# Kernel optimization log

Hardware: AMD Instinct MI355X
Metric: run time of the kernel (lower is better)

## Reference

```python
import jax, jax.numpy as jnp
import numpy as np

B, N, D, H, S = 4, 32768, 256, 8, 64
DH = D // H  # 32


def setup_inputs() -> dict:
    key = jax.random.key(0)
    ks = jax.random.split(key, 8)
    s = 0.02
    return {
        "x": jax.random.normal(ks[0], (B, N, D), jnp.float32),
        "W_fx": jax.random.normal(ks[1], (D, D), jnp.float32) * s,
        "b_fx": jnp.zeros((D,), jnp.float32),
        "W_x": jax.random.normal(ks[2], (D, D), jnp.float32) * s,
        "b_x": jnp.zeros((D,), jnp.float32),
        "W_slice": jax.random.normal(ks[3], (DH, S), jnp.float32) * s,
        "b_slice": jnp.zeros((S,), jnp.float32),
        "temperature": jnp.full((1, H, 1, 1), 0.5, jnp.float32),
        "W_qkv": jax.random.normal(ks[4], (DH, 3 * DH), jnp.float32) * s,  # qkv_bias=False
        "W_out": jax.random.normal(ks[5], (D, D), jnp.float32) * s,
        "b_out": jnp.zeros((D,), jnp.float32),
    }


def reference(x, W_fx, b_fx, W_x, b_x, W_slice, b_slice, temperature, W_qkv, W_out, b_out):
    b, n, d = x.shape
    h, dh = H, d // H
    scale = dh ** -0.5
    # per-head projections: [b, h, n, dh]
    fx_mid = (x @ W_fx + b_fx).reshape(b, n, h, dh).transpose(0, 2, 1, 3)
    x_mid = (x @ W_x + b_x).reshape(b, n, h, dh).transpose(0, 2, 1, 3)
    # soft slice assignment: softmax over slices [b, h, n, s]
    logits = (x_mid @ W_slice + b_slice) / temperature
    slice_weights = jax.nn.softmax(logits, axis=-1)
    slice_norm = slice_weights.sum(axis=2)  # [b, h, s]
    # weighted pooling of points into slice tokens [b, h, s, dh]
    slice_token = jnp.einsum('bhnc,bhns->bhsc', fx_mid, slice_weights)
    slice_token = slice_token / (slice_norm[..., None] + 1e-5)
    # tiny attention among slice tokens
    q, k, v = jnp.split(slice_token @ W_qkv, 3, axis=-1)
    dots = jnp.einsum('bhsc,bhtc->bhst', q, k) * scale
    attn = jax.nn.softmax(dots, axis=-1)
    out_slice_token = attn @ v  # [b, h, s, dh]
    # scatter back to points [b, h, n, dh]
    out_x = jnp.einsum('bhsc,bhns->bhnc', out_slice_token, slice_weights)
    out_x = out_x.transpose(0, 2, 1, 3).reshape(b, n, d)
    return out_x @ W_out + b_out
```

## Files before the change

kernel.cpp:

```cpp
#include <hip/hip_runtime.h>
#include <math.h>

#define TS_N 32768
#define TS_M 131072

typedef short bf16x8 __attribute__((ext_vector_type(8)));
typedef float f32x4  __attribute__((ext_vector_type(4)));
typedef unsigned short us4 __attribute__((ext_vector_type(4)));
typedef unsigned short us8 __attribute__((ext_vector_type(8)));

static __device__ __forceinline__ unsigned short f2bf(float f) {
    unsigned u = __float_as_uint(f);
    u = u + 0x7FFF + ((u >> 16) & 1);
    return (unsigned short)(u >> 16);
}
static __device__ __forceinline__ float bf2f(unsigned short b) {
    return __uint_as_float(((unsigned)b) << 16);
}

#define GL16(gp, lp) __builtin_amdgcn_global_load_lds( \
    (const __attribute__((address_space(1))) unsigned int*)(gp), \
    (__attribute__((address_space(3))) unsigned int*)(lp), 16, 0, 0)

__global__ __launch_bounds__(256) void k0_split(
    const float* __restrict__ src, unsigned short* __restrict__ h,
    unsigned short* __restrict__ l, int n4)
{
    for (int i = blockIdx.x * 256 + threadIdx.x; i < n4; i += gridDim.x * 256) {
        float4 v = ((const float4*)src)[i];
        us4 vh, vl;
        float c[4] = {v.x, v.y, v.z, v.w};
#pragma unroll
        for (int j = 0; j < 4; ++j) {
            unsigned short hh = f2bf(c[j]);
            vh[j] = hh;
            vl[j] = f2bf(c[j] - bf2f(hh));
        }
        ((us4*)h)[i] = vh;
        ((us4*)l)[i] = vl;
    }
}

__global__ __launch_bounds__(256) void k0_wt(
    const float* __restrict__ Wfx, const float* __restrict__ Wx,
    unsigned short* __restrict__ Wth, unsigned short* __restrict__ Wtl)
{
    const int n = blockIdx.x;
    const int wsel = blockIdx.y;
    const int k = threadIdx.x;
    const float v = (wsel ? Wx : Wfx)[k * 256 + n];
    const unsigned short hh = f2bf(v);
    const int idx = (wsel * 256 + n) * 256 + k;
    Wth[idx] = hh;
    Wtl[idx] = f2bf(v - bf2f(hh));
}

template<int K>
static __device__ __forceinline__ void gemm_body(
    const unsigned short* __restrict__ Ah, const unsigned short* __restrict__ Al,
    const unsigned short* __restrict__ Bth, const unsigned short* __restrict__ Btl,
    const float* __restrict__ bias, float* __restrict__ OUT,
    int row0, int n0)
{
    __shared__ unsigned short Alds[2][128 * 32];
    __shared__ unsigned short Blds[2][128 * 32];
    const int t = threadIdx.x;
    const int w = t >> 6, l = t & 63;
    const int wm = w >> 1, wn = w & 1;
    const int lr = l & 15, lk = l >> 4;

    f32x4 acc[4][4];
#pragma unroll
    for (int i = 0; i < 4; ++i)
#pragma unroll
        for (int j = 0; j < 4; ++j) {
            acc[i][j][0] = 0.f; acc[i][j][1] = 0.f;
            acc[i][j][2] = 0.f; acc[i][j][3] = 0.f;
        }

    const int NSTEP = K / 32;
    for (int step = 0; step < NSTEP; ++step) {
        const int kk = step * 32;
        if (step > 0) __syncthreads();
#pragma unroll
        for (int g2i = 0; g2i < 2; ++g2i) {
            const int g2 = w + g2i * 4;
            const size_t ar = (size_t)(row0 + g2 * 16 + lr) * K + kk + lk * 8;
            const size_t br = (size_t)(g2 * 16 + lr) * K + kk + lk * 8;
            const int lb = g2 * 64 * 8;
            GL16(Ah + ar, &Alds[0][lb]);
            GL16(Al + ar, &Alds[1][lb]);
            GL16(Bth + br, &Blds[0][lb]);
            GL16(Btl + br, &Blds[1][lb]);
        }
        __syncthreads();

        bf16x8 ah[4], al[4], bh[4], bl[4];
#pragma unroll
        for (int g = 0; g < 4; ++g) {
            const int ac = (((wm * 4 + g) * 4 + lk) * 16 + lr) * 8;
            ah[g] = *(const bf16x8*)&Alds[0][ac];
            al[g] = *(const bf16x8*)&Alds[1][ac];
            const int bc = (((wn * 4 + g) * 4 + lk) * 16 + lr) * 8;
            bh[g] = *(const bf16x8*)&Blds[0][bc];
            bl[g] = *(const bf16x8*)&Blds[1][bc];
        }
#pragma unroll
        for (int m = 0; m < 4; ++m)
#pragma unroll
            for (int n = 0; n < 4; ++n) {
                acc[m][n] = __builtin_amdgcn_mfma_f32_16x16x32_bf16(ah[m], bh[n], acc[m][n], 0, 0, 0);
                acc[m][n] = __builtin_amdgcn_mfma_f32_16x16x32_bf16(ah[m], bl[n], acc[m][n], 0, 0, 0);
                acc[m][n] = __builtin_amdgcn_mfma_f32_16x16x32_bf16(al[m], bh[n], acc[m][n], 0, 0, 0);
            }
    }

    float bv[4];
#pragma unroll
    for (int n = 0; n < 4; ++n) bv[n] = bias[n0 + wn * 64 + n * 16 + lr];
#pragma unroll
    for (int m = 0; m < 4; ++m)
#pragma unroll
        for (int n = 0; n < 4; ++n) {
            const int col = n0 + wn * 64 + n * 16 + lr;
#pragma unroll
            for (int r = 0; r < 4; ++r) {
                const int row = row0 + wm * 64 + m * 16 + lk * 4 + r;
                OUT[(size_t)row * 256 + col] = acc[m][n][r] + bv[n];
            }
        }
}

__global__ __launch_bounds__(256) void k1_gemm(
    const unsigned short* __restrict__ Ah, const unsigned short* __restrict__ Al,
    const unsigned short* __restrict__ Wth, const unsigned short* __restrict__ Wtl,
    const float* __restrict__ bfx, const float* __restrict__ bx,
    float* __restrict__ FX, float* __restrict__ XM)
{
    const int L = blockIdx.x;
    const int xcd = L & 7, ii = L >> 3;
    const int rb = xcd * 128 + (ii >> 2), nsel = ii & 3;
    const int row0 = rb * 128;
    const int n0 = (nsel & 1) * 128;
    const unsigned short* Bth = Wth + (nsel >> 1) * 65536 + n0 * 256;
    const unsigned short* Btl = Wtl + (nsel >> 1) * 65536 + n0 * 256;
    const float* bias = (nsel >> 1) ? bx : bfx;
    float* OUT = (nsel >> 1) ? XM : FX;
    gemm_body<256>(Ah, Al, Bth, Btl, bias, OUT, row0, n0);
}

__global__ __launch_bounds__(256) void k4_gemm(
    const unsigned short* __restrict__ SWh, const unsigned short* __restrict__ SWl,
    const unsigned short* __restrict__ Gth, const unsigned short* __restrict__ Gtl,
    const float* __restrict__ bout, float* __restrict__ out)
{
    const int L = blockIdx.x;
    const int xcd = L & 7, ii = L >> 3;
    const int rb = xcd * 128 + (ii >> 1), nsel = ii & 1;
    const int row0 = rb * 128;
    const int n0 = nsel * 128;
    const int b = row0 >> 15;
    const unsigned short* Bth = Gth + ((size_t)b * 256 + n0) * 512;
    const unsigned short* Btl = Gtl + ((size_t)b * 256 + n0) * 512;
    gemm_body<512>(SWh, SWl, Bth, Btl, bout, out, row0, n0);
}

__global__ __launch_bounds__(256) void k1b_slice_softmax(
    const float* __restrict__ XM, const float* __restrict__ Wsl,
    const float* __restrict__ bsl, const float* __restrict__ temp,
    unsigned short* __restrict__ SWh, unsigned short* __restrict__ SWl)
{
    __shared__ float XMs[32][68];
    __shared__ float Ws[32][68];
    __shared__ float Ls[64][68];
    const int t  = threadIdx.x;
    const int r0 = blockIdx.x * 64;
    const int h  = blockIdx.y;

    {
        const int m = t >> 2, cq = (t & 3) * 8;
        float4 v0 = *(const float4*)&XM[(size_t)(r0 + m) * 256 + h * 32 + cq];
        float4 v1 = *(const float4*)&XM[(size_t)(r0 + m) * 256 + h * 32 + cq + 4];
        XMs[cq + 0][m] = v0.x; XMs[cq + 1][m] = v0.y; XMs[cq + 2][m] = v0.z; XMs[cq + 3][m] = v0.w;
        XMs[cq + 4][m] = v1.x; XMs[cq + 5][m] = v1.y; XMs[cq + 6][m] = v1.z; XMs[cq + 7][m] = v1.w;
        const int wk = t >> 3, wn = (t & 7) * 8;
        float4 u0 = *(const float4*)&Wsl[wk * 64 + wn];
        float4 u1 = *(const float4*)&Wsl[wk * 64 + wn + 4];
        *(float4*)&Ws[wk][wn]     = u0;
        *(float4*)&Ws[wk][wn + 4] = u1;
    }
    __syncthreads();

    const int tx = t & 15, ty = t >> 4;
    float acc[4][4];
#pragma unroll
    for (int i = 0; i < 4; ++i)
#pragma unroll
        for (int j = 0; j < 4; ++j) acc[i][j] = 0.f;
#pragma unroll
    for (int c = 0; c < 32; ++c) {
        float4 av = *(const float4*)&XMs[c][ty * 4];
        float4 bv = *(const float4*)&Ws[c][tx * 4];
        float a_[4] = {av.x, av.y, av.z, av.w};
        float b_[4] = {bv.x, bv.y, bv.z, bv.w};
#pragma unroll
        for (int i = 0; i < 4; ++i)
#pragma unroll
            for (int j = 0; j < 4; ++j)
                acc[i][j] = fmaf(a_[i], b_[j], acc[i][j]);
    }
    const float invt = 1.0f / temp[h];
#pragma unroll
    for (int i = 0; i < 4; ++i)
#pragma unroll
        for (int j = 0; j < 4; ++j)
            Ls[ty * 4 + i][tx * 4 + j] = (acc[i][j] + bsl[tx * 4 + j]) * invt;
    __syncthreads();

    const int row = t >> 2, j4 = t & 3;
    float v[16];
    float mx = -1e30f;
#pragma unroll
    for (int i = 0; i < 16; ++i) { v[i] = Ls[row][j4 * 16 + i]; mx = fmaxf(mx, v[i]); }
    mx = fmaxf(mx, __shfl_xor(mx, 1));
    mx = fmaxf(mx, __shfl_xor(mx, 2));
    float sum = 0.f;
#pragma unroll
    for (int i = 0; i < 16; ++i) { v[i] = expf(v[i] - mx); sum += v[i]; }
    sum += __shfl_xor(sum, 1);
    sum += __shfl_xor(sum, 2);
    const float inv = 1.0f / sum;
#pragma unroll
    for (int q = 0; q < 4; ++q) {
        us4 oh, ol;
#pragma unroll
        for (int j = 0; j < 4; ++j) {
            const float o = v[q * 4 + j] * inv;
            const unsigned short hh = f2bf(o);
            oh[j] = hh;
            ol[j] = f2bf(o - bf2f(hh));
        }
        const size_t idx = (size_t)(r0 + row) * 512 + h * 64 + j4 * 16 + q * 4;
        *(us4*)&SWh[idx] = oh;
        *(us4*)&SWl[idx] = ol;
    }
}

__global__ __launch_bounds__(256) void k2_pool(
    const float* __restrict__ FX,
    const unsigned short* __restrict__ SWh, const unsigned short* __restrict__ SWl,
    float* __restrict__ PART, float* __restrict__ PARTN)
{
    __shared__ float SWs[2][64][68];
    __shared__ float FXs[2][64][36];
    const int t = threadIdx.x;
    const int chunk = blockIdx.x;
    const int bh = blockIdx.y;
    const int b = bh >> 3, h = bh & 7;
    const int gbase = b * TS_N + chunk * 512;

    const int rs = t >> 2;
    const int ch0 = t & 3;

    us8 swh[2], swl[2];
    float4 fxr[2];

    {
        const size_t swbase = (size_t)(gbase + rs) * 512 + h * 64;
        swh[0] = *(const us8*)&SWh[swbase + ch0 * 8];
        swh[1] = *(const us8*)&SWh[swbase + (ch0 + 4) * 8];
        swl[0] = *(const us8*)&SWl[swbase + ch0 * 8];
        swl[1] = *(const us8*)&SWl[swbase + (ch0 + 4) * 8];
        const size_t fxbase = (size_t)(gbase + rs) * 256 + h * 32;
        fxr[0] = *(const float4*)&FX[fxbase + ch0 * 4];
        fxr[1] = *(const float4*)&FX[fxbase + (ch0 + 4) * 4];
    }

    const int c = t & 31, sb = (t >> 5) * 8;
    float acc[8];
#pragma unroll
    for (int j = 0; j < 8; ++j) acc[j] = 0.f;
    float accn = 0.f;
    int buf = 0;

    for (int s = 0; s < 8; ++s) {
#pragma unroll
        for (int q = 0; q < 2; ++q) {
            const int cq = (ch0 + q * 4) * 8;
#pragma unroll
            for (int j = 0; j < 8; ++j)
                SWs[buf][rs][cq + j] = bf2f(swh[q][j]) + bf2f(swl[q][j]);
            *(float4*)&FXs[buf][rs][(ch0 + q * 4) * 4] = fxr[q];
        }
        __syncthreads();
        if (s < 7) {
            const int g2 = gbase + (s + 1) * 64 + rs;
            const size_t swbase = (size_t)g2 * 512 + h * 64;
            swh[0] = *(const us8*)&SWh[swbase + ch0 * 8];
            swh[1] = *(const us8*)&SWh[swbase + (ch0 + 4) * 8];
            swl[0] = *(const us8*)&SWl[swbase + ch0 * 8];
            swl[1] = *(const us8*)&SWl[swbase + (ch0 + 4) * 8];
            const size_t fxbase = (size_t)g2 * 256 + h * 32;
            fxr[0] = *(const float4*)&FX[fxbase + ch0 * 4];
            fxr[1] = *(const float4*)&FX[fxbase + (ch0 + 4) * 4];
        }
#pragma unroll 8
        for (int rr = 0; rr < 64; ++rr) {
            const float f = FXs[buf][rr][c];
            float4 s0 = *(const float4*)&SWs[buf][rr][sb];
            float4 s1 = *(const float4*)&SWs[buf][rr][sb + 4];
            acc[0] = fmaf(f, s0.x, acc[0]); acc[1] = fmaf(f, s0.y, acc[1]);
            acc[2] = fmaf(f, s0.z, acc[2]); acc[3] = fmaf(f, s0.w, acc[3]);
            acc[4] = fmaf(f, s1.x, acc[4]); acc[5] = fmaf(f, s1.y, acc[5]);
            acc[6] = fmaf(f, s1.z, acc[6]); acc[7] = fmaf(f, s1.w, acc[7]);
        }
        if (t < 64) {
#pragma unroll 8
            for (int rr = 0; rr < 64; ++rr) accn += SWs[buf][rr][t];
        }
        buf ^= 1;
    }

    const int pbase = (bh * 64 + chunk) * 2048;
#pragma unroll
    for (int j = 0; j < 8; ++j) PART[pbase + (sb + j) * 32 + c] = acc[j];
    if (t < 64) PARTN[(bh * 64 + chunk) * 64 + t] = accn;
}

__global__ __launch_bounds__(256) void k2b_reduce(
    const float* __restrict__ PART, const float* __restrict__ PARTN,
    float* __restrict__ ST, float* __restrict__ NORM)
{
    const int g = blockIdx.x, bh = blockIdx.y, t = threadIdx.x;
    const int e = g * 256 + t;
    float s = 0.f;
    for (int ch = 0; ch < 64; ++ch) s += PART[(size_t)(bh * 64 + ch) * 2048 + e];
    ST[bh * 2048 + e] = s;
    if (g == 0 && t < 64) {
        float sn = 0.f;
        for (int ch = 0; ch < 64; ++ch) sn += PARTN[(bh * 64 + ch) * 64 + t];
        NORM[bh * 64 + t] = sn;
    }
}

__global__ __launch_bounds__(64) void k3_attn(
    const float* __restrict__ ST, const float* __restrict__ NORM,
    const float* __restrict__ Wqkv, float* __restrict__ OST)
{
    __shared__ float Wq[32 * 96];
    __shared__ float Kl[64][32];
    __shared__ float Vl[64][32];
    __shared__ float Dl[64][68];
    const int bh = blockIdx.x;
    const int s  = threadIdx.x;

    for (int i = 0; i < 48; ++i) Wq[i * 64 + s] = Wqkv[i * 64 + s];
    float st[32];
    const float nrm = NORM[bh * 64 + s] + 1e-5f;
#pragma unroll
    for (int c = 0; c < 32; ++c) st[c] = ST[bh * 2048 + s * 32 + c] / nrm;
    __syncthreads();

    float q[32];
#pragma unroll
    for (int o4 = 0; o4 < 8; ++o4) {
        float ax = 0.f, ay = 0.f, az = 0.f, aw = 0.f;
#pragma unroll
        for (int c = 0; c < 32; ++c) {
            float4 w = *(const float4*)&Wq[c * 96 + o4 * 4];
            ax = fmaf(st[c], w.x, ax); ay = fmaf(st[c], w.y, ay);
            az = fmaf(st[c], w.z, az); aw = fmaf(st[c], w.w, aw);
        }
        q[o4 * 4 + 0] = ax; q[o4 * 4 + 1] = ay; q[o4 * 4 + 2] = az; q[o4 * 4 + 3] = aw;
    }
#pragma unroll
    for (int o4 = 0; o4 < 8; ++o4) {
        float ax = 0.f, ay = 0.f, az = 0.f, aw = 0.f;
#pragma unroll
        for (int c = 0; c < 32; ++c) {
            float4 w = *(const float4*)&Wq[c * 96 + 32 + o4 * 4];
            ax = fmaf(st[c], w.x, ax); ay = fmaf(st[c], w.y, ay);
            az = fmaf(st[c], w.z, az); aw = fmaf(st[c], w.w, aw);
        }
        float4 kv; kv.x = ax; kv.y = ay; kv.z = az; kv.w = aw;
        *(float4*)&Kl[s][o4 * 4] = kv;
    }
#pragma unroll
    for (int o4 = 0; o4 < 8; ++o4) {
        float ax = 0.f, ay = 0.f, az = 0.f, aw = 0.f;
#pragma unroll
        for (int c = 0; c < 32; ++c) {
            float4 w = *(const float4*)&Wq[c * 96 + 64 + o4 * 4];
            ax = fmaf(st[c], w.x, ax); ay = fmaf(st[c], w.y, ay);
            az = fmaf(st[c], w.z, az); aw = fmaf(st[c], w.w, aw);
        }
        float4 vv; vv.x = ax; vv.y = ay; vv.z = az; vv.w = aw;
        *(float4*)&Vl[s][o4 * 4] = vv;
    }
    __syncthreads();

    const float scale = 0.17677669529663687f;
    float mx = -1e30f;
    for (int t2 = 0; t2 < 64; ++t2) {
        float d = 0.f;
#pragma unroll
        for (int c4 = 0; c4 < 8; ++c4) {
            float4 kv = *(const float4*)&Kl[t2][c4 * 4];
            d = fmaf(q[c4 * 4 + 0], kv.x, d); d = fmaf(q[c4 * 4 + 1], kv.y, d);
            d = fmaf(q[c4 * 4 + 2], kv.z, d); d = fmaf(q[c4 * 4 + 3], kv.w, d);
        }
        d *= scale;
        Dl[s][t2] = d;
        mx = fmaxf(mx, d);
    }
    float sum = 0.f;
    for (int t2 = 0; t2 < 64; ++t2) { float e = expf(Dl[s][t2] - mx); Dl[s][t2] = e; sum += e; }
    const float inv = 1.0f / sum;
    float out[32];
#pragma unroll
    for (int c = 0; c < 32; ++c) out[c] = 0.f;
    for (int t2 = 0; t2 < 64; ++t2) {
        const float p = Dl[s][t2] * inv;
#pragma unroll
        for (int c4 = 0; c4 < 8; ++c4) {
            float4 vv = *(const float4*)&Vl[t2][c4 * 4];
            out[c4 * 4 + 0] = fmaf(p, vv.x, out[c4 * 4 + 0]);
            out[c4 * 4 + 1] = fmaf(p, vv.y, out[c4 * 4 + 1]);
            out[c4 * 4 + 2] = fmaf(p, vv.z, out[c4 * 4 + 2]);
            out[c4 * 4 + 3] = fmaf(p, vv.w, out[c4 * 4 + 3]);
        }
    }
#pragma unroll
    for (int c4 = 0; c4 < 8; ++c4) {
        float4 ov;
        ov.x = out[c4 * 4 + 0]; ov.y = out[c4 * 4 + 1];
        ov.z = out[c4 * 4 + 2]; ov.w = out[c4 * 4 + 3];
        *(float4*)&OST[bh * 2048 + s * 32 + c4 * 4] = ov;
    }
}

__global__ __launch_bounds__(256) void k3b_precomb(
    const float* __restrict__ OST, const float* __restrict__ Wout,
    unsigned short* __restrict__ Gth, unsigned short* __restrict__ Gtl)
{
    __shared__ float OSTs[64][36];
    __shared__ float Wc[32][256];
    const int bh = blockIdx.x;
    const int b = bh >> 3, h = bh & 7;
    const int t = threadIdx.x;

#pragma unroll
    for (int j = 0; j < 2; ++j) {
        const int e = (j * 256 + t) * 4;
        float4 v = *(const float4*)&OST[bh * 2048 + e];
        const int s = e >> 5, c = e & 31;
        OSTs[s][c + 0] = v.x; OSTs[s][c + 1] = v.y;
        OSTs[s][c + 2] = v.z; OSTs[s][c + 3] = v.w;
    }
#pragma unroll
    for (int j = 0; j < 8; ++j) {
        const int e = (j * 256 + t) * 4;
        const int c = e >> 8, o = e & 255;
        *(float4*)&Wc[c][o] = *(const float4*)&Wout[(h * 32 + c) * 256 + o];
    }
    __syncthreads();

    float wcol[32];
#pragma unroll
    for (int c = 0; c < 32; ++c) wcol[c] = Wc[c][t];

    for (int s = 0; s < 64; ++s) {
        float a = 0.f;
#pragma unroll
        for (int c = 0; c < 32; ++c) a = fmaf(OSTs[s][c], wcol[c], a);
        const unsigned short gh = f2bf(a);
        const size_t idx = ((size_t)(b * 256 + t)) * 512 + h * 64 + s;
        Gth[idx] = gh;
        Gtl[idx] = f2bf(a - bf2f(gh));
    }
}

extern "C" void kernel_launch(void* const* d_in, const int* in_sizes, int n_in,
                              void* d_out, int out_size, void* d_ws, size_t ws_size,
                              hipStream_t stream) {
    (void)in_sizes; (void)n_in; (void)out_size; (void)ws_size;
    const float* x    = (const float*)d_in[0];
    const float* Wfx  = (const float*)d_in[1];
    const float* bfx  = (const float*)d_in[2];
    const float* Wx   = (const float*)d_in[3];
    const float* bx   = (const float*)d_in[4];
    const float* Wsl  = (const float*)d_in[5];
    const float* bsl  = (const float*)d_in[6];
    const float* temp = (const float*)d_in[7];
    const float* Wqkv = (const float*)d_in[8];
    const float* Wout = (const float*)d_in[9];
    const float* bout = (const float*)d_in[10];
    float* out = (float*)d_out;
    char* w = (char*)d_ws;

    float* XM = (float*)w;
    char* sh = w + 134217728;
    unsigned short* Xh  = (unsigned short*)sh;
    unsigned short* Xl  = Xh + 33554432;
    unsigned short* SWh = (unsigned short*)sh;
    unsigned short* SWl = SWh + 67108864;
    char* p = w + 134217728 + 268435456;
    p += 8388608;
    p += 262144;
    float* ST    = (float*)p;            p += 262144;
    float* NORM  = (float*)p;            p += 8192;
    float* OST   = (float*)p;            p += 262144;
    unsigned short* Gth = (unsigned short*)p; p += 1048576;
    unsigned short* Gtl = (unsigned short*)p; p += 1048576;
    unsigned short* Wth = (unsigned short*)p; p += 262144;
    unsigned short* Wtl = (unsigned short*)p; p += 262144;
    float* PART  = XM;
    float* PARTN = XM + 4194304;
    float* FX = out;

    k0_split<<<2048, 256, 0, stream>>>(x, Xh, Xl, TS_M * 256 / 4);
    k0_wt<<<dim3(256, 2), 256, 0, stream>>>(Wfx, Wx, Wth, Wtl);
    k1_gemm<<<4096, 256, 0, stream>>>(Xh, Xl, Wth, Wtl, bfx, bx, FX, XM);
    k1b_slice_softmax<<<dim3(TS_M / 64, 8), 256, 0, stream>>>(XM, Wsl, bsl, temp, SWh, SWl);
    k2_pool<<<dim3(64, 32), 256, 0, stream>>>(FX, SWh, SWl, PART, PARTN);
    k2b_reduce<<<dim3(8, 32), 256, 0, stream>>>(PART, PARTN, ST, NORM);
    k3_attn<<<32, 64, 0, stream>>>(ST, NORM, Wqkv, OST);
    k3b_precomb<<<32, 256, 0, stream>>>(OST, Wout, Gth, Gtl);
    k4_gemm<<<2048, 256, 0, stream>>>(SWh, SWl, Gth, Gtl, bout, out);
}
```

Measured before the change: 675.4 us.

## Fuse x bf16 split and slice softmax into the projection GEMM

The separate pass that splits x into hi/lo bf16 is removed; the GEMM now loads fp32 x directly and converts it to hi/lo in registers before writing to LDS. The slice-logit projection and softmax are moved into the GEMM epilogue for the x_mid tiles, through an LDS transpose, so the x_mid intermediate is never written to or read back from global memory. This removes two kernel launches and several large HBM round trips. In exchange the GEMM does synchronous fp32 loads and conversion instead of async global-to-LDS copies, and the epilogue keeps large per-thread register arrays that may lower occupancy or spill.

```diff
diff --git a/kernel.cpp b/kernel.cpp
--- a/kernel.cpp
+++ b/kernel.cpp
@@ -21,25 +21,6 @@
 #define GL16(gp, lp) __builtin_amdgcn_global_load_lds( \
     (const __attribute__((address_space(1))) unsigned int*)(gp), \
     (__attribute__((address_space(3))) unsigned int*)(lp), 16, 0, 0)
-
-__global__ __launch_bounds__(256) void k0_split(
-    const float* __restrict__ src, unsigned short* __restrict__ h,
-    unsigned short* __restrict__ l, int n4)
-{
-    for (int i = blockIdx.x * 256 + threadIdx.x; i < n4; i += gridDim.x * 256) {
-        float4 v = ((const float4*)src)[i];
-        us4 vh, vl;
-        float c[4] = {v.x, v.y, v.z, v.w};
-#pragma unroll
-        for (int j = 0; j < 4; ++j) {
-            unsigned short hh = f2bf(c[j]);
-            vh[j] = hh;
-            vl[j] = f2bf(c[j] - bf2f(hh));
-        }
-        ((us4*)h)[i] = vh;
-        ((us4*)l)[i] = vl;
-    }
-}
 
 __global__ __launch_bounds__(256) void k0_wt(
     const float* __restrict__ Wfx, const float* __restrict__ Wx,
@@ -55,88 +36,23 @@
     Wtl[idx] = f2bf(v - bf2f(hh));
 }
 
-template<int K>
-static __device__ __forceinline__ void gemm_body(
-    const unsigned short* __restrict__ Ah, const unsigned short* __restrict__ Al,
-    const unsigned short* __restrict__ Bth, const unsigned short* __restrict__ Btl,
-    const float* __restrict__ bias, float* __restrict__ OUT,
-    int row0, int n0)
-{
-    __shared__ unsigned short Alds[2][128 * 32];
-    __shared__ unsigned short Blds[2][128 * 32];
-    const int t = threadIdx.x;
-    const int w = t >> 6, l = t & 63;
-    const int wm = w >> 1, wn = w & 1;
-    const int lr = l & 15, lk = l >> 4;
-
-    f32x4 acc[4][4];
-#pragma unroll
-    for (int i = 0; i < 4; ++i)
-#pragma unroll
-        for (int j = 0; j < 4; ++j) {
-            acc[i][j][0] = 0.f; acc[i][j][1] = 0.f;
-            acc[i][j][2] = 0.f; acc[i][j][3] = 0.f;
-        }
-
-    const int NSTEP = K / 32;
-    for (int step = 0; step < NSTEP; ++step) {
-        const int kk = step * 32;
-        if (step > 0) __syncthreads();
-#pragma unroll
-        for (int g2i = 0; g2i < 2; ++g2i) {
-            const int g2 = w + g2i * 4;
-            const size_t ar = (size_t)(row0 + g2 * 16 + lr) * K + kk + lk * 8;
-            const size_t br = (size_t)(g2 * 16 + lr) * K + kk + lk * 8;
-            const int lb = g2 * 64 * 8;
-            GL16(Ah + ar, &Alds[0][lb]);
-            GL16(Al + ar, &Alds[1][lb]);
-            GL16(Bth + br, &Blds[0][lb]);
-            GL16(Btl + br, &Blds[1][lb]);
-        }
-        __syncthreads();
-
-        bf16x8 ah[4], al[4], bh[4], bl[4];
-#pragma unroll
-        for (int g = 0; g < 4; ++g) {
-            const int ac = (((wm * 4 + g) * 4 + lk) * 16 + lr) * 8;
-            ah[g] = *(const bf16x8*)&Alds[0][ac];
-            al[g] = *(const bf16x8*)&Alds[1][ac];
-            const int bc = (((wn * 4 + g) * 4 + lk) * 16 + lr) * 8;
-            bh[g] = *(const bf16x8*)&Blds[0][bc];
-            bl[g] = *(const bf16x8*)&Blds[1][bc];
-        }
-#pragma unroll
-        for (int m = 0; m < 4; ++m)
-#pragma unroll
-            for (int n = 0; n < 4; ++n) {
-                acc[m][n] = __builtin_amdgcn_mfma_f32_16x16x32_bf16(ah[m], bh[n], acc[m][n], 0, 0, 0);
-                acc[m][n] = __builtin_amdgcn_mfma_f32_16x16x32_bf16(ah[m], bl[n], acc[m][n], 0, 0, 0);
-                acc[m][n] = __builtin_amdgcn_mfma_f32_16x16x32_bf16(al[m], bh[n], acc[m][n], 0, 0, 0);
-            }
-    }
-
-    float bv[4];
-#pragma unroll
-    for (int n = 0; n < 4; ++n) bv[n] = bias[n0 + wn * 64 + n * 16 + lr];
-#pragma unroll
-    for (int m = 0; m < 4; ++m)
-#pragma unroll
-        for (int n = 0; n < 4; ++n) {
-            const int col = n0 + wn * 64 + n * 16 + lr;
-#pragma unroll
-            for (int r = 0; r < 4; ++r) {
-                const int row = row0 + wm * 64 + m * 16 + lk * 4 + r;
-                OUT[(size_t)row * 256 + col] = acc[m][n][r] + bv[n];
-            }
-        }
-}
-
 __global__ __launch_bounds__(256) void k1_gemm(
-    const unsigned short* __restrict__ Ah, const unsigned short* __restrict__ Al,
+    const float* __restrict__ x,
     const unsigned short* __restrict__ Wth, const unsigned short* __restrict__ Wtl,
     const float* __restrict__ bfx, const float* __restrict__ bx,
-    float* __restrict__ FX, float* __restrict__ XM)
-{
+    const float* __restrict__ Wsl, const float* __restrict__ bsl,
+    const float* __restrict__ temp,
+    float* __restrict__ FX,
+    unsigned short* __restrict__ SWh, unsigned short* __restrict__ SWl)
+{
+    __shared__ char U[34816];
+    __shared__ float Wsls[2048];
+    unsigned short* AldsH = (unsigned short*)U;
+    unsigned short* AldsL = AldsH + 4096;
+    unsigned short* BldsH = AldsL + 4096;
+    unsigned short* BldsL = BldsH + 4096;
+    float* XT = (float*)U;
+
     const int L = blockIdx.x;
     const int xcd = L & 7, ii = L >> 3;
     const int rb = xcd * 128 + (ii >> 2), nsel = ii & 3;
@@ -144,9 +60,158 @@
     const int n0 = (nsel & 1) * 128;
     const unsigned short* Bth = Wth + (nsel >> 1) * 65536 + n0 * 256;
     const unsigned short* Btl = Wtl + (nsel >> 1) * 65536 + n0 * 256;
-    const float* bias = (nsel >> 1) ? bx : bfx;
-    float* OUT = (nsel >> 1) ? XM : FX;
-    gemm_body<256>(Ah, Al, Bth, Btl, bias, OUT, row0, n0);
+
+    const int t = threadIdx.x;
+    const int w = t >> 6, l = t & 63;
+    const int wm = w >> 1, wn = w & 1;
+    const int lr = l & 15, lk = l >> 4;
+
+    if (nsel >= 2) {
+#pragma unroll
+        for (int j = 0; j < 8; ++j) Wsls[j * 256 + t] = Wsl[j * 256 + t];
+    }
+
+    f32x4 acc[4][4];
+#pragma unroll
+    for (int i = 0; i < 4; ++i)
+#pragma unroll
+        for (int j = 0; j < 4; ++j) {
+            acc[i][j][0] = 0.f; acc[i][j][1] = 0.f;
+            acc[i][j][2] = 0.f; acc[i][j][3] = 0.f;
+        }
+
+    for (int step = 0; step < 8; ++step) {
+        const int kk = step * 32;
+        if (step > 0) __syncthreads();
+#pragma unroll
+        for (int g2i = 0; g2i < 2; ++g2i) {
+            const int g2 = w + g2i * 4;
+            const size_t br = (size_t)(g2 * 16 + lr) * 256 + kk + lk * 8;
+            const int lb = g2 * 512;
+            GL16(Bth + br, BldsH + lb);
+            GL16(Btl + br, BldsL + lb);
+        }
+#pragma unroll
+        for (int g2i = 0; g2i < 2; ++g2i) {
+            const int g2 = w + g2i * 4;
+            const float* ap = &x[(size_t)(row0 + g2 * 16 + lr) * 256 + kk + lk * 8];
+            float4 a0 = *(const float4*)ap;
+            float4 a1 = *(const float4*)(ap + 4);
+            float cc[8] = {a0.x, a0.y, a0.z, a0.w, a1.x, a1.y, a1.z, a1.w};
+            us8 vh, vl;
+#pragma unroll
+            for (int j = 0; j < 8; ++j) {
+                const unsigned short hb = f2bf(cc[j]);
+                vh[j] = hb;
+                vl[j] = f2bf(cc[j] - bf2f(hb));
+            }
+            *(us8*)&AldsH[(g2 * 64 + l) * 8] = vh;
+            *(us8*)&AldsL[(g2 * 64 + l) * 8] = vl;
+        }
+        __syncthreads();
+
+        bf16x8 ah[4], al[4], bh[4], bl[4];
+#pragma unroll
+        for (int g = 0; g < 4; ++g) {
+            const int ac = (((wm * 4 + g) * 4 + lk) * 16 + lr) * 8;
+            ah[g] = *(const bf16x8*)&AldsH[ac];
+            al[g] = *(const bf16x8*)&AldsL[ac];
+            const int bc = (((wn * 4 + g) * 4 + lk) * 16 + lr) * 8;
+            bh[g] = *(const bf16x8*)&BldsH[bc];
+            bl[g] = *(const bf16x8*)&BldsL[bc];
+        }
+#pragma unroll
+        for (int m = 0; m < 4; ++m)
+#pragma unroll
+            for (int n = 0; n < 4; ++n) {
+                acc[m][n] = __builtin_amdgcn_mfma_f32_16x16x32_bf16(ah[m], bh[n], acc[m][n], 0, 0, 0);
+                acc[m][n] = __builtin_amdgcn_mfma_f32_16x16x32_bf16(ah[m], bl[n], acc[m][n], 0, 0, 0);
+                acc[m][n] = __builtin_amdgcn_mfma_f32_16x16x32_bf16(al[m], bh[n], acc[m][n], 0, 0, 0);
+            }
+    }
+
+    if (nsel < 2) {
+        float bv[4];
+#pragma unroll
+        for (int n = 0; n < 4; ++n) bv[n] = bfx[n0 + wn * 64 + n * 16 + lr];
+#pragma unroll
+        for (int m = 0; m < 4; ++m)
+#pragma unroll
+            for (int n = 0; n < 4; ++n) {
+                const int col = n0 + wn * 64 + n * 16 + lr;
+#pragma unroll
+                for (int r = 0; r < 4; ++r) {
+                    const int row = row0 + wm * 64 + m * 16 + lk * 4 + r;
+                    FX[(size_t)row * 256 + col] = acc[m][n][r] + bv[n];
+                }
+            }
+        return;
+    }
+
+    float bv[4];
+#pragma unroll
+    for (int n = 0; n < 4; ++n) bv[n] = bx[n0 + wn * 64 + n * 16 + lr];
+
+    for (int hh = 0; hh < 2; ++hh) {
+        __syncthreads();
+        if (wm == hh) {
+#pragma unroll
+            for (int m = 0; m < 4; ++m)
+#pragma unroll
+                for (int n = 0; n < 4; ++n)
+#pragma unroll
+                    for (int r = 0; r < 4; ++r)
+                        XT[(wn * 64 + n * 16 + lr) * 66 + m * 16 + lk * 4 + r] =
+                            acc[m][n][r] + bv[n];
+        }
+        __syncthreads();
+
+        const int h4 = w;
+        const int row = l;
+        const int hg = (n0 >> 5) + h4;
+        float xm[32];
+#pragma unroll
+        for (int c = 0; c < 32; ++c) xm[c] = XT[(h4 * 32 + c) * 66 + row];
+        const float invt = 1.0f / temp[hg];
+
+        float lg[64];
+        float mx = -1e30f;
+#pragma unroll
+        for (int sb = 0; sb < 16; ++sb) {
+            float4 a = *(const float4*)&bsl[sb * 4];
+#pragma unroll
+            for (int c = 0; c < 32; ++c) {
+                const float4 wv = *(const float4*)&Wsls[c * 64 + sb * 4];
+                a.x = fmaf(xm[c], wv.x, a.x);
+                a.y = fmaf(xm[c], wv.y, a.y);
+                a.z = fmaf(xm[c], wv.z, a.z);
+                a.w = fmaf(xm[c], wv.w, a.w);
+            }
+            float v0 = a.x * invt, v1 = a.y * invt, v2 = a.z * invt, v3 = a.w * invt;
+            lg[sb * 4 + 0] = v0; lg[sb * 4 + 1] = v1;
+            lg[sb * 4 + 2] = v2; lg[sb * 4 + 3] = v3;
+            mx = fmaxf(mx, fmaxf(fmaxf(v0, v1), fmaxf(v2, v3)));
+        }
+        float sum = 0.f;
+#pragma unroll
+        for (int s = 0; s < 64; ++s) { lg[s] = expf(lg[s] - mx); sum += lg[s]; }
+        const float inv = 1.0f / sum;
+
+        const size_t base = (size_t)(row0 + hh * 64 + row) * 512 + hg * 64;
+#pragma unroll
+        for (int sc = 0; sc < 8; ++sc) {
+            us8 oh, ol;
+#pragma unroll
+            for (int j = 0; j < 8; ++j) {
+                const float o = lg[sc * 8 + j] * inv;
+                const unsigned short hb = f2bf(o);
+                oh[j] = hb;
+                ol[j] = f2bf(o - bf2f(hb));
+            }
+            *(us8*)&SWh[base + sc * 8] = oh;
+            *(us8*)&SWl[base + sc * 8] = ol;
+        }
+    }
 }
 
 __global__ __launch_bounds__(256) void k4_gemm(
@@ -154,6 +219,8 @@
     const unsigned short* __restrict__ Gth, const unsigned short* __restrict__ Gtl,
     const float* __restrict__ bout, float* __restrict__ out)
 {
+    __shared__ unsigned short Alds[2][128 * 32];
+    __shared__ unsigned short Blds[2][128 * 32];
     const int L = blockIdx.x;
     const int xcd = L & 7, ii = L >> 3;
     const int rb = xcd * 128 + (ii >> 1), nsel = ii & 1;
@@ -162,88 +229,71 @@
     const int b = row0 >> 15;
     const unsigned short* Bth = Gth + ((size_t)b * 256 + n0) * 512;
     const unsigned short* Btl = Gtl + ((size_t)b * 256 + n0) * 512;
-    gemm_body<512>(SWh, SWl, Bth, Btl, bout, out, row0, n0);
-}
-
-__global__ __launch_bounds__(256) void k1b_slice_softmax(
-    const float* __restrict__ XM, const float* __restrict__ Wsl,
-    const float* __restrict__ bsl, const float* __restrict__ temp,
-    unsigned short* __restrict__ SWh, unsigned short* __restrict__ SWl)
-{
-    __shared__ float XMs[32][68];
-    __shared__ float Ws[32][68];
-    __shared__ float Ls[64][68];
-    const int t  = threadIdx.x;
-    const int r0 = blockIdx.x * 64;
-    const int h  = blockIdx.y;
-
-    {
-        const int m = t >> 2, cq = (t & 3) * 8;
-        float4 v0 = *(const float4*)&XM[(size_t)(r0 + m) * 256 + h * 32 + cq];
-        float4 v1 = *(const float4*)&XM[(size_t)(r0 + m) * 256 + h * 32 + cq + 4];
-        XMs[cq + 0][m] = v0.x; XMs[cq + 1][m] = v0.y; XMs[cq + 2][m] = v0.z; XMs[cq + 3][m] = v0.w;
-        XMs[cq + 4][m] = v1.x; XMs[cq + 5][m] = v1.y; XMs[cq + 6][m] = v1.z; XMs[cq + 7][m] = v1.w;
-        const int wk = t >> 3, wn = (t & 7) * 8;
-        float4 u0 = *(const float4*)&Wsl[wk * 64 + wn];
-        float4 u1 = *(const float4*)&Wsl[wk * 64 + wn + 4];
-        *(float4*)&Ws[wk][wn]     = u0;
-        *(float4*)&Ws[wk][wn + 4] = u1;
-    }
-    __syncthreads();
-
-    const int tx = t & 15, ty = t >> 4;
-    float acc[4][4];
+
+    const int t = threadIdx.x;
+    const int w = t >> 6, l = t & 63;
+    const int wm = w >> 1, wn = w & 1;
+    const int lr = l & 15, lk = l >> 4;
+
+    f32x4 acc[4][4];
 #pragma unroll
     for (int i = 0; i < 4; ++i)
 #pragma unroll
-        for (int j = 0; j < 4; ++j) acc[i][j] = 0.f;
-#pragma unroll
-    for (int c = 0; c < 32; ++c) {
-        float4 av = *(const float4*)&XMs[c][ty * 4];
-        float4 bv = *(const float4*)&Ws[c][tx * 4];
-        float a_[4] = {av.x, av.y, av.z, av.w};
-        float b_[4] = {bv.x, bv.y, bv.z, bv.w};
-#pragma unroll
-        for (int i = 0; i < 4; ++i)
-#pragma unroll
-            for (int j = 0; j < 4; ++j)
-                acc[i][j] = fmaf(a_[i], b_[j], acc[i][j]);
-    }
-    const float invt = 1.0f / temp[h];
-#pragma unroll
-    for (int i = 0; i < 4; ++i)
-#pragma unroll
-        for (int j = 0; j < 4; ++j)
-            Ls[ty * 4 + i][tx * 4 + j] = (acc[i][j] + bsl[tx * 4 + j]) * invt;
-    __syncthreads();
-
-    const int row = t >> 2, j4 = t & 3;
-    float v[16];
-    float mx = -1e30f;
-#pragma unroll
-    for (int i = 0; i < 16; ++i) { v[i] = Ls[row][j4 * 16 + i]; mx = fmaxf(mx, v[i]); }
-    mx = fmaxf(mx, __shfl_xor(mx, 1));
-    mx = fmaxf(mx, __shfl_xor(mx, 2));
-    float sum = 0.f;
-#pragma unroll
-    for (int i = 0; i < 16; ++i) { v[i] = expf(v[i] - mx); sum += v[i]; }
-    sum += __shfl_xor(sum, 1);
-    sum += __shfl_xor(sum, 2);
-    const float inv = 1.0f / sum;
-#pragma unroll
-    for (int q = 0; q < 4; ++q) {
-        us4 oh, ol;
-#pragma unroll
         for (int j = 0; j < 4; ++j) {
-            const float o = v[q * 4 + j] * inv;
-            const unsigned short hh = f2bf(o);
-            oh[j] = hh;
-            ol[j] = f2bf(o - bf2f(hh));
-        }
-        const size_t idx = (size_t)(r0 + row) * 512 + h * 64 + j4 * 16 + q * 4;
-        *(us4*)&SWh[idx] = oh;
-        *(us4*)&SWl[idx] = ol;
-    }
+            acc[i][j][0] = 0.f; acc[i][j][1] = 0.f;
+            acc[i][j][2] = 0.f; acc[i][j][3] = 0.f;
+        }
+
+    for (int step = 0; step < 16; ++step) {
+        const int kk = step * 32;
+        if (step > 0) __syncthreads();
+#pragma unroll
+        for (int g2i = 0; g2i < 2; ++g2i) {
+            const int g2 = w + g2i * 4;
+            const size_t ar = (size_t)(row0 + g2 * 16 + lr) * 512 + kk + lk * 8;
+            const size_t br = (size_t)(g2 * 16 + lr) * 512 + kk + lk * 8;
+            const int lb = g2 * 512;
+            GL16(SWh + ar, &Alds[0][lb]);
+            GL16(SWl + ar, &Alds[1][lb]);
+            GL16(Bth + br, &Blds[0][lb]);
+            GL16(Btl + br, &Blds[1][lb]);
+        }
+        __syncthreads();
+
+        bf16x8 ah[4], al[4], bh[4], bl[4];
+#pragma unroll
+        for (int g = 0; g < 4; ++g) {
+            const int ac = (((wm * 4 + g) * 4 + lk) * 16 + lr) * 8;
+            ah[g] = *(const bf16x8*)&Alds[0][ac];
+            al[g] = *(const bf16x8*)&Alds[1][ac];
+            const int bc = (((wn * 4 + g) * 4 + lk) * 16 + lr) * 8;
+            bh[g] = *(const bf16x8*)&Blds[0][bc];
+            bl[g] = *(const bf16x8*)&Blds[1][bc];
+        }
+#pragma unroll
+        for (int m = 0; m < 4; ++m)
+#pragma unroll
+            for (int n = 0; n < 4; ++n) {
+                acc[m][n] = __builtin_amdgcn_mfma_f32_16x16x32_bf16(ah[m], bh[n], acc[m][n], 0, 0, 0);
+                acc[m][n] = __builtin_amdgcn_mfma_f32_16x16x32_bf16(ah[m], bl[n], acc[m][n], 0, 0, 0);
+                acc[m][n] = __builtin_amdgcn_mfma_f32_16x16x32_bf16(al[m], bh[n], acc[m][n], 0, 0, 0);
+            }
+    }
+
+    float bv[4];
+#pragma unroll
+    for (int n = 0; n < 4; ++n) bv[n] = bout[n0 + wn * 64 + n * 16 + lr];
+#pragma unroll
+    for (int m = 0; m < 4; ++m)
+#pragma unroll
+        for (int n = 0; n < 4; ++n) {
+            const int col = n0 + wn * 64 + n * 16 + lr;
+#pragma unroll
+            for (int r = 0; r < 4; ++r) {
+                const int row = row0 + wm * 64 + m * 16 + lk * 4 + r;
+                out[(size_t)row * 256 + col] = acc[m][n][r] + bv[n];
+            }
+        }
 }
 
 __global__ __launch_bounds__(256) void k2_pool(
@@ -498,15 +548,11 @@
     float* out = (float*)d_out;
     char* w = (char*)d_ws;
 
-    float* XM = (float*)w;
-    char* sh = w + 134217728;
-    unsigned short* Xh  = (unsigned short*)sh;
-    unsigned short* Xl  = Xh + 33554432;
-    unsigned short* SWh = (unsigned short*)sh;
+    unsigned short* SWh = (unsigned short*)w;
     unsigned short* SWl = SWh + 67108864;
-    char* p = w + 134217728 + 268435456;
-    p += 8388608;
-    p += 262144;
+    char* p = w + 268435456;
+    float* PART  = (float*)p;            p += 16777216;
+    float* PARTN = (float*)p;            p += 524288;
     float* ST    = (float*)p;            p += 262144;
     float* NORM  = (float*)p;            p += 8192;
     float* OST   = (float*)p;            p += 262144;
@@ -514,14 +560,11 @@
     unsigned short* Gtl = (unsigned short*)p; p += 1048576;
     unsigned short* Wth = (unsigned short*)p; p += 262144;
     unsigned short* Wtl = (unsigned short*)p; p += 262144;
-    float* PART  = XM;
-    float* PARTN = XM + 4194304;
     float* FX = out;
 
-    k0_split<<<2048, 256, 0, stream>>>(x, Xh, Xl, TS_M * 256 / 4);
     k0_wt<<<dim3(256, 2), 256, 0, stream>>>(Wfx, Wx, Wth, Wtl);
-    k1_gemm<<<4096, 256, 0, stream>>>(Xh, Xl, Wth, Wtl, bfx, bx, FX, XM);
-    k1b_slice_softmax<<<dim3(TS_M / 64, 8), 256, 0, stream>>>(XM, Wsl, bsl, temp, SWh, SWl);
+    k1_gemm<<<4096, 256, 0, stream>>>(x, Wth, Wtl, bfx, bx, Wsl, bsl, temp,
+                                      FX, SWh, SWl);
     k2_pool<<<dim3(64, 32), 256, 0, stream>>>(FX, SWh, SWl, PART, PARTN);
     k2b_reduce<<<dim3(8, 32), 256, 0, stream>>>(PART, PARTN, ST, NORM);
     k3_attn<<<32, 64, 0, stream>>>(ST, NORM, Wqkv, OST);
```

New measurement: 1.293 ms. 1.91x slower.
